# Performance work log

Measured on AMD Instinct MI355X. Metric: run time of the kernel, lower is better.

The kernel has to match this reference:

```python
import jax, jax.numpy as jnp
import numpy as np

N_NODES = 50000
HEADS = 4
OUT_DIM = 64
NEG_SLOPE = 0.2
BETA = 0.5
C_CONST = 1.0
EPS = 1e-16


def setup_inputs() -> dict:
    key = jax.random.key(0)
    ks = jax.random.split(key, 6)
    in_dim = 128
    x = jax.random.normal(ks[0], (N_NODES, in_dim), dtype=jnp.float32)
    edge_index = jax.random.randint(ks[1], (2, 800000), 0, N_NODES, dtype=jnp.int64)
    # GATConv params (glorot-ish scale)
    W = jax.random.normal(ks[2], (in_dim, HEADS * OUT_DIM), dtype=jnp.float32) * (1.0 / np.sqrt(in_dim))
    att_src = jax.random.normal(ks[3], (HEADS, OUT_DIM), dtype=jnp.float32) * (1.0 / np.sqrt(OUT_DIM))
    att_dst = jax.random.normal(ks[4], (HEADS, OUT_DIM), dtype=jnp.float32) * (1.0 / np.sqrt(OUT_DIM))
    bias = jnp.zeros((HEADS * OUT_DIM,), dtype=jnp.float32)
    return {"x": x, "edge_index": edge_index, "W": W, "att_src": att_src,
            "att_dst": att_dst, "bias": bias}


def _gat_conv(x, edge_index, W, att_src, att_dst, bias):
    N = x.shape[0]
    # add self loops (PyG GATConv default)
    loop = jnp.arange(N, dtype=edge_index.dtype)
    src = jnp.concatenate([edge_index[0], loop])
    dst = jnp.concatenate([edge_index[1], loop])
    # linear transform: [N, H, F]
    h = (x @ W).reshape(N, HEADS, OUT_DIM)
    # per-node attention logits: [N, H]
    a_src = jnp.einsum('nhf,hf->nh', h, att_src)
    a_dst = jnp.einsum('nhf,hf->nh', h, att_dst)
    # per-edge logits and segment softmax over destination nodes
    e = jax.nn.leaky_relu(a_src[src] + a_dst[dst], negative_slope=NEG_SLOPE)  # [E, H]
    m = jax.ops.segment_max(e, dst, num_segments=N)                           # [N, H]
    ex = jnp.exp(e - m[dst])
    s = jax.ops.segment_sum(ex, dst, num_segments=N)                          # [N, H]
    alpha = ex / (s[dst] + EPS)                                               # [E, H]
    # aggregate messages: [N, H, F]
    out = jax.ops.segment_sum(alpha[:, :, None] * h[src], dst, num_segments=N)
    return out.reshape(N, HEADS * OUT_DIM) + bias


def reference(x, edge_index, W, att_src, att_dst, bias):
    # eval mode: feature dropout and attention dropout are identity
    z = _gat_conv(x, edge_index, W, att_src, att_dst, bias)
    return BETA * z + (C_CONST - BETA) * jax.nn.elu(z)
```

## Files before the change

### kernel.cpp

```cpp
#include <hip/hip_runtime.h>
#include <hip/hip_bf16.h>

typedef unsigned short u16;
typedef __attribute__((ext_vector_type(8))) short bf16x8;
typedef __attribute__((ext_vector_type(4))) float f32x4;

#define HEADS 4
#define OUT_DIM 64
#define HF 256
#define IN_DIM 128
#define NEG_SLOPE 0.2f
#define EPSF 1e-16f

__device__ __forceinline__ float braw2f(u16 u) {
    union { float f; unsigned int i; } c; c.i = ((unsigned int)u) << 16; return c.f;
}
__device__ __forceinline__ u16 f2braw(float v) {
    __hip_bfloat16 t = __float2bfloat16(v);
    return *(u16*)&t;
}
__device__ __forceinline__ float lrelu(float e) { return e < 0.f ? NEG_SLOPE * e : e; }

__device__ __forceinline__ bool detect_i64(const int* ei) {
    return (ei[1] | ei[3] | ei[5] | ei[7] | ei[9] | ei[11] | ei[13] | ei[15]) == 0;
}
__device__ __forceinline__ void get_edge(const int* ei, int E, int t, bool i64,
                                         int& s, int& d) {
    if (t < E) {
        if (i64) { s = ei[2 * t]; d = ei[2 * (E + t)]; }
        else     { s = ei[t];     d = ei[E + t]; }
    } else {
        s = d = t - E;
    }
}

__global__ __launch_bounds__(256) void init_kernel(const float* __restrict__ W,
                                                   const float* __restrict__ att_s,
                                                   const float* __restrict__ att_d,
                                                   float* __restrict__ wa_s,
                                                   float* __restrict__ wa_d,
                                                   int* __restrict__ cnt4,
                                                   int* __restrict__ cur,
                                                   int* __restrict__ gcnt,
                                                   int* __restrict__ hist,
                                                   int* __restrict__ bcur,
                                                   int N, int NZ) {
    int b = blockIdx.x;
    if (b == 0) {
        if (threadIdx.x == 0) *gcnt = 0;
        hist[threadIdx.x] = 0;
        bcur[threadIdx.x] = 0;
    }
    if (b < NZ) {
        int i = b * 256 + threadIdx.x;
        if (i < N) {
            cnt4[i] = 0;
            cnt4[N + i] = 0;
            cnt4[2 * N + i] = 0;
            cnt4[3 * N + i] = 0;
            cur[i] = 0;
        }
    } else {
        for (int idx = threadIdx.x; idx < HEADS * IN_DIM; idx += 256) {
            int h = idx >> 7, k = idx & 127;
            float ss = 0.f, sd = 0.f;
            for (int f = 0; f < OUT_DIM; ++f) {
                float wv = W[k * HF + h * OUT_DIM + f];
                ss = fmaf(wv, att_s[h * OUT_DIM + f], ss);
                sd = fmaf(wv, att_d[h * OUT_DIM + f], sd);
            }
            wa_s[idx] = ss;
            wa_d[idx] = sd;
        }
    }
}

__global__ __launch_bounds__(256) void phase1_kernel(const float* __restrict__ x,
                                                     const int* __restrict__ ei,
                                                     const float* __restrict__ W,
                                                     const float* __restrict__ wa_s,
                                                     const float* __restrict__ wa_d,
                                                     float* __restrict__ a_src,
                                                     float* __restrict__ a_dst,
                                                     u16* __restrict__ xb,
                                                     u16* __restrict__ Wfrag,
                                                     int* __restrict__ cnt4,
                                                     int N, int E, int NA, int NC) {
    int b = blockIdx.x;
    if (b < NA) {
        int wid = threadIdx.x >> 6;
        int l = threadIdx.x & 63;
        int g = l >> 4, c = l & 15, kc = c * 8;
        int v = b * 16 + wid * 4 + g;
        if (v >= N) return;

        const float4* xr = (const float4*)(x + (size_t)v * IN_DIM + kc);
        float4 x0 = xr[0], x1 = xr[1];

        uint4 u;
        u.x = (unsigned)f2braw(x0.x) | ((unsigned)f2braw(x0.y) << 16);
        u.y = (unsigned)f2braw(x0.z) | ((unsigned)f2braw(x0.w) << 16);
        u.z = (unsigned)f2braw(x1.x) | ((unsigned)f2braw(x1.y) << 16);
        u.w = (unsigned)f2braw(x1.z) | ((unsigned)f2braw(x1.w) << 16);
        *(uint4*)(xb + (size_t)v * IN_DIM + kc) = u;

        float ps[4], pd[4];
        #pragma unroll
        for (int h = 0; h < 4; ++h) {
            const float4* s4 = (const float4*)(wa_s + h * IN_DIM + kc);
            const float4* d4 = (const float4*)(wa_d + h * IN_DIM + kc);
            float4 s0 = s4[0], s1 = s4[1], d0 = d4[0], d1 = d4[1];
            ps[h] = x0.x*s0.x + x0.y*s0.y + x0.z*s0.z + x0.w*s0.w
                  + x1.x*s1.x + x1.y*s1.y + x1.z*s1.z + x1.w*s1.w;
            pd[h] = x0.x*d0.x + x0.y*d0.y + x0.z*d0.z + x0.w*d0.w
                  + x1.x*d1.x + x1.y*d1.y + x1.z*d1.z + x1.w*d1.w;
        }
        #pragma unroll
        for (int off = 1; off < 16; off <<= 1) {
            #pragma unroll
            for (int h = 0; h < 4; ++h) {
                ps[h] += __shfl_xor(ps[h], off);
                pd[h] += __shfl_xor(pd[h], off);
            }
        }
        if (c == 0) {
            float4 vs, vd;
            vs.x = ps[0]; vs.y = ps[1]; vs.z = ps[2]; vs.w = ps[3];
            vd.x = pd[0]; vd.y = pd[1]; vd.z = pd[2]; vd.w = pd[3];
            *(float4*)(a_src + (size_t)v * HEADS) = vs;
            *(float4*)(a_dst + (size_t)v * HEADS) = vd;
        }
    } else if (b < NA + NC) {
        int t = (b - NA) * 256 + threadIdx.x;
        if (t >= E + N) return;
        bool i64 = detect_i64(ei);
        int src, dst; get_edge(ei, E, t, i64, src, dst);
        if (src >= 0 && src < N && dst >= 0 && dst < N)
            atomicAdd(cnt4 + (t & 3) * N + dst, 1);
    } else {
        int bb = b - NA - NC;
        for (int idx = bb * 256 + threadIdx.x; idx < 32768; idx += 8 * 256) {
            int j = idx & 7, l = (idx >> 3) & 63, t = (idx >> 9) & 3;
            int s = (idx >> 11) & 3, h = (idx >> 13) & 3;
            int k = s * 32 + ((l >> 4) & 3) * 8 + j;
            int col = h * OUT_DIM + t * 16 + (l & 15);
            Wfrag[idx] = f2braw(W[k * HF + col]);
        }
    }
}

__global__ __launch_bounds__(256) void offset_kernel(int* __restrict__ cnt4,
                                                     int* __restrict__ offs,
                                                     int* __restrict__ gcnt,
                                                     int* __restrict__ hist, int N) {
    __shared__ int lh[256];
    lh[threadIdx.x] = 0;
    __syncthreads();

    int idx = blockIdx.x * 256 + threadIdx.x;
    int l = threadIdx.x & 63;
    int d = 0;
    if (idx < N) {
        d = cnt4[idx] + cnt4[N + idx] + cnt4[2 * N + idx] + cnt4[3 * N + idx];
        cnt4[idx] = d;
        atomicAdd(lh + min(max(d, 0), 255), 1);
    }

    int s = d;
    #pragma unroll
    for (int off = 1; off < 64; off <<= 1) {
        int t = __shfl_up(s, off);
        if (l >= off) s += t;
    }
    int base = 0;
    if (l == 63) base = atomicAdd(gcnt, s);
    base = __shfl(base, 63);
    if (idx < N) offs[idx] = base + s - d;

    __syncthreads();
    if (lh[threadIdx.x]) atomicAdd(hist + threadIdx.x, lh[threadIdx.x]);
}

__global__ __launch_bounds__(256) void fillscatter_kernel(const int* __restrict__ ei,
                                                          const int* __restrict__ offs,
                                                          int* __restrict__ cur,
                                                          int* __restrict__ slots,
                                                          uint2* __restrict__ wslots,
                                                          const float* __restrict__ a_src,
                                                          const float* __restrict__ a_dst,
                                                          const int* __restrict__ cnt,
                                                          const int* __restrict__ hist,
                                                          int* __restrict__ bcur,
                                                          int* __restrict__ perm,
                                                          int E, int N, int NC) {
    __shared__ int sc[256];
    __shared__ int lh[256];
    __shared__ int lbase[256];

    int b = blockIdx.x;
    if (b < NC) {
        int t = b * 256 + threadIdx.x;
        if (t >= E + N) return;
        bool i64 = detect_i64(ei);
        int src, dst; get_edge(ei, E, t, i64, src, dst);
        if (src >= 0 && src < N && dst >= 0 && dst < N) {
            int pos = atomicAdd(cur + dst, 1);
            int idx = offs[dst] + pos;
            slots[idx] = src;
            if (wslots) {
                float4 as = ((const float4*)a_src)[src];
                float4 ad = ((const float4*)a_dst)[dst];
                float w0 = __expf(lrelu(as.x + ad.x));
                float w1 = __expf(lrelu(as.y + ad.y));
                float w2 = __expf(lrelu(as.z + ad.z));
                float w3 = __expf(lrelu(as.w + ad.w));
                uint2 wp;
                wp.x = (unsigned)f2braw(w0) | ((unsigned)f2braw(w1) << 16);
                wp.y = (unsigned)f2braw(w2) | ((unsigned)f2braw(w3) << 16);
                wslots[idx] = wp;
            }
        }
    } else {
        int tid = threadIdx.x;
        sc[tid] = hist[tid];
        lh[tid] = 0;
        __syncthreads();
        #pragma unroll
        for (int off = 1; off < 256; off <<= 1) {
            int tv = (tid >= off) ? sc[tid - off] : 0;
            __syncthreads();
            sc[tid] += tv;
            __syncthreads();
        }

        int idx = (b - NC) * 256 + tid;
        int bk = 0, mypos = 0;
        bool valid = (idx < N);
        if (valid) {
            bk = min(max(cnt[idx], 0), 255);
            mypos = atomicAdd(lh + bk, 1);
        }
        __syncthreads();
        int c = lh[tid];
        if (c) lbase[tid] = atomicAdd(bcur + tid, c);
        __syncthreads();
        if (valid) {
            int p = (N - sc[bk]) + lbase[bk] + mypos;
            if (p >= 0 && p < N) perm[p] = idx;
        }
    }
}

#define ACC_EDGE(wp, r) do { \
    float w0_ = braw2f((wp).x & 0xffff), w1_ = braw2f((wp).x >> 16); \
    float w2_ = braw2f((wp).y & 0xffff), w3_ = braw2f((wp).y >> 16); \
    ls0 += w0_; ls1 += w1_; ls2 += w2_; ls3 += w3_; \
    float xv_[8]; \
    xv_[0] = braw2f((r).x & 0xffff); xv_[1] = braw2f((r).x >> 16); \
    xv_[2] = braw2f((r).y & 0xffff); xv_[3] = braw2f((r).y >> 16); \
    xv_[4] = braw2f((r).z & 0xffff); xv_[5] = braw2f((r).z >> 16); \
    xv_[6] = braw2f((r).w & 0xffff); xv_[7] = braw2f((r).w >> 16); \
    _Pragma("unroll") \
    for (int q_ = 0; q_ < 8; ++q_) { \
        G0[q_] = fmaf(w0_, xv_[q_], G0[q_]); \
        G1[q_] = fmaf(w1_, xv_[q_], G1[q_]); \
        G2[q_] = fmaf(w2_, xv_[q_], G2[q_]); \
        G3[q_] = fmaf(w3_, xv_[q_], G3[q_]); \
    } \
} while (0)

__global__ __launch_bounds__(256) void fused_gz_kernel(const int* __restrict__ perm,
                                                       const int* __restrict__ offs,
                                                       const int* __restrict__ cnt,
                                                       const int* __restrict__ slots,
                                                       const uint2* __restrict__ wslots,
                                                       const u16* __restrict__ xb,
                                                       const u16* __restrict__ Wfrag,
                                                       const float* __restrict__ bias,
                                                       float* __restrict__ out,
                                                       int N, int ET) {
    __shared__ u16 smem[16 * 520];
    __shared__ int pvals[16];

    int tid = threadIdx.x;
    int wid = tid >> 6;
    int l = tid & 63;
    int g = l >> 4, c = l & 15, kc = c * 8;
    int n = wid * 4 + g;
    int pidx = blockIdx.x * 16 + n;

    int v = -1;
    if (pidx < N) {
        v = perm[pidx];
        if (v < 0 || v >= N) v = -1;
    }
    if (c == 0) pvals[n] = v;

    int beg = 0, end = 0;
    if (v >= 0) {
        beg = offs[v];
        int deg = cnt[v];
        beg = max(0, min(beg, ET));
        end = max(beg, min(beg + deg, ET));
    }

    float ls0 = 0.f, ls1 = 0.f, ls2 = 0.f, ls3 = 0.f;
    float G0[8] = {0,0,0,0,0,0,0,0};
    float G1[8] = {0,0,0,0,0,0,0,0};
    float G2[8] = {0,0,0,0,0,0,0,0};
    float G3[8] = {0,0,0,0,0,0,0,0};

    int j = beg;
    for (; j + 4 <= end; j += 4) {
        int s0 = max(0, min(slots[j],     N - 1));
        int s1 = max(0, min(slots[j + 1], N - 1));
        int s2 = max(0, min(slots[j + 2], N - 1));
        int s3 = max(0, min(slots[j + 3], N - 1));
        uint2 wp0 = wslots[j];
        uint2 wp1 = wslots[j + 1];
        uint2 wp2 = wslots[j + 2];
        uint2 wp3 = wslots[j + 3];
        uint4 r0 = *(const uint4*)(xb + (size_t)s0 * IN_DIM + kc);
        uint4 r1 = *(const uint4*)(xb + (size_t)s1 * IN_DIM + kc);
        uint4 r2 = *(const uint4*)(xb + (size_t)s2 * IN_DIM + kc);
        uint4 r3 = *(const uint4*)(xb + (size_t)s3 * IN_DIM + kc);
        ACC_EDGE(wp0, r0);
        ACC_EDGE(wp1, r1);
        ACC_EDGE(wp2, r2);
        ACC_EDGE(wp3, r3);
    }
    for (; j < end; ++j) {
        int s0 = max(0, min(slots[j], N - 1));
        uint2 wp0 = wslots[j];
        uint4 r0 = *(const uint4*)(xb + (size_t)s0 * IN_DIM + kc);
        ACC_EDGE(wp0, r0);
    }

    if (v >= 0) {
        float i0 = 1.f / (ls0 + EPSF), i1 = 1.f / (ls1 + EPSF);
        float i2 = 1.f / (ls2 + EPSF), i3 = 1.f / (ls3 + EPSF);
        u16* lp = smem + n * 520 + c * 8;
        #pragma unroll
        for (int h = 0; h < 4; ++h) {
            const float* G = h == 0 ? G0 : h == 1 ? G1 : h == 2 ? G2 : G3;
            float inv = h == 0 ? i0 : h == 1 ? i1 : h == 2 ? i2 : i3;
            uint4 u;
            u.x = (unsigned)f2braw(G[0] * inv) | ((unsigned)f2braw(G[1] * inv) << 16);
            u.y = (unsigned)f2braw(G[2] * inv) | ((unsigned)f2braw(G[3] * inv) << 16);
            u.z = (unsigned)f2braw(G[4] * inv) | ((unsigned)f2braw(G[5] * inv) << 16);
            u.w = (unsigned)f2braw(G[6] * inv) | ((unsigned)f2braw(G[7] * inv) << 16);
            *(uint4*)(lp + h * 128) = u;
        }
    } else {
        u16* lp = smem + n * 520 + c * 8;
        uint4 z = {0, 0, 0, 0};
        #pragma unroll
        for (int h = 0; h < 4; ++h) *(uint4*)(lp + h * 128) = z;
    }
    __syncthreads();

    int h = wid;
    int q = l >> 4, mcol = l & 15;

    const u16* lp = smem + mcol * 520 + h * 128 + q * 8;
    bf16x8 A[4];
    A[0] = *(const bf16x8*)(lp);
    A[1] = *(const bf16x8*)(lp + 32);
    A[2] = *(const bf16x8*)(lp + 64);
    A[3] = *(const bf16x8*)(lp + 96);

    f32x4 acc0 = {0.f,0.f,0.f,0.f}, acc1 = acc0, acc2 = acc0, acc3 = acc0;
    #pragma unroll
    for (int s = 0; s < 4; ++s) {
        const u16* wb = Wfrag + (((h * 4 + s) * 4) << 9) + l * 8;
        bf16x8 B0 = *(const bf16x8*)(wb);
        bf16x8 B1 = *(const bf16x8*)(wb + 512);
        bf16x8 B2 = *(const bf16x8*)(wb + 1024);
        bf16x8 B3 = *(const bf16x8*)(wb + 1536);
        acc0 = __builtin_amdgcn_mfma_f32_16x16x32_bf16(A[s], B0, acc0, 0, 0, 0);
        acc1 = __builtin_amdgcn_mfma_f32_16x16x32_bf16(A[s], B1, acc1, 0, 0, 0);
        acc2 = __builtin_amdgcn_mfma_f32_16x16x32_bf16(A[s], B2, acc2, 0, 0, 0);
        acc3 = __builtin_amdgcn_mfma_f32_16x16x32_bf16(A[s], B3, acc3, 0, 0, 0);
    }

    #pragma unroll
    for (int bt = 0; bt < 4; ++bt) {
        f32x4 a = bt == 0 ? acc0 : bt == 1 ? acc1 : bt == 2 ? acc2 : acc3;
        float b = bias[h * OUT_DIM + bt * 16 + mcol];
        #pragma unroll
        for (int r = 0; r < 4; ++r) {
            int vv = pvals[q * 4 + r];
            if (vv >= 0) {
                float z = a[r] + b;
                float y = z > 0.f ? z : 0.5f * z + 0.5f * (__expf(z) - 1.f);
                out[(size_t)vv * HF + h * OUT_DIM + bt * 16 + mcol] = y;
            }
        }
    }
}

__global__ __launch_bounds__(512) void gather_bf_kernel(const int* __restrict__ offs,
                                                        const int* __restrict__ cnt,
                                                        const int* __restrict__ slots,
                                                        const u16* __restrict__ xb,
                                                        const float* __restrict__ a_src,
                                                        const float* __restrict__ a_dst,
                                                        u16* __restrict__ Gout, int N, int ET) {
    int v = (blockIdx.x * 512 + threadIdx.x) >> 6;
    int l = threadIdx.x & 63;
    if (v >= N) return;
    int h = l >> 4, c = l & 15, kc = c * 8;

    int beg = offs[v];
    int deg = cnt[v];
    beg = max(0, min(beg, ET));
    int end = max(beg, min(beg + deg, ET));
    float adh = a_dst[v * HEADS + h];

    float ls = 0.f;
    float G[8] = {0.f,0.f,0.f,0.f,0.f,0.f,0.f,0.f};

    int j = beg;
    for (; j + 4 <= end; j += 4) {
        int s0 = max(0, min(slots[j],     N - 1));
        int s1 = max(0, min(slots[j + 1], N - 1));
        int s2 = max(0, min(slots[j + 2], N - 1));
        int s3 = max(0, min(slots[j + 3], N - 1));
        float w0 = __expf(lrelu(a_src[s0 * HEADS + h] + adh));
        float w1 = __expf(lrelu(a_src[s1 * HEADS + h] + adh));
        float w2 = __expf(lrelu(a_src[s2 * HEADS + h] + adh));
        float w3 = __expf(lrelu(a_src[s3 * HEADS + h] + adh));
        uint4 r0 = *(const uint4*)(xb + (size_t)s0 * IN_DIM + kc);
        uint4 r1 = *(const uint4*)(xb + (size_t)s1 * IN_DIM + kc);
        uint4 r2 = *(const uint4*)(xb + (size_t)s2 * IN_DIM + kc);
        uint4 r3 = *(const uint4*)(xb + (size_t)s3 * IN_DIM + kc);
        ls += (w0 + w1) + (w2 + w3);
        unsigned ua[4];
        ua[0]=r0.x; ua[1]=r0.y; ua[2]=r0.z; ua[3]=r0.w;
        #pragma unroll
        for (int q = 0; q < 4; ++q) {
            G[2*q]   = fmaf(w0, braw2f(ua[q] & 0xffff), G[2*q]);
            G[2*q+1] = fmaf(w0, braw2f(ua[q] >> 16),    G[2*q+1]);
        }
        ua[0]=r1.x; ua[1]=r1.y; ua[2]=r1.z; ua[3]=r1.w;
        #pragma unroll
        for (int q = 0; q < 4; ++q) {
            G[2*q]   = fmaf(w1, braw2f(ua[q] & 0xffff), G[2*q]);
            G[2*q+1] = fmaf(w1, braw2f(ua[q] >> 16),    G[2*q+1]);
        }
        ua[0]=r2.x; ua[1]=r2.y; ua[2]=r2.z; ua[3]=r2.w;
        #pragma unroll
        for (int q = 0; q < 4; ++q) {
            G[2*q]   = fmaf(w2, braw2f(ua[q] & 0xffff), G[2*q]);
            G[2*q+1] = fmaf(w2, braw2f(ua[q] >> 16),    G[2*q+1]);
        }
        ua[0]=r3.x; ua[1]=r3.y; ua[2]=r3.z; ua[3]=r3.w;
        #pragma unroll
        for (int q = 0; q < 4; ++q) {
            G[2*q]   = fmaf(w3, braw2f(ua[q] & 0xffff), G[2*q]);
            G[2*q+1] = fmaf(w3, braw2f(ua[q] >> 16),    G[2*q+1]);
        }
    }
    for (; j < end; ++j) {
        int s0 = max(0, min(slots[j], N - 1));
        float w0 = __expf(lrelu(a_src[s0 * HEADS + h] + adh));
        uint4 r0 = *(const uint4*)(xb + (size_t)s0 * IN_DIM + kc);
        ls += w0;
        unsigned ua[4]; ua[0]=r0.x; ua[1]=r0.y; ua[2]=r0.z; ua[3]=r0.w;
        #pragma unroll
        for (int q = 0; q < 4; ++q) {
            G[2*q]   = fmaf(w0, braw2f(ua[q] & 0xffff), G[2*q]);
            G[2*q+1] = fmaf(w0, braw2f(ua[q] >> 16),    G[2*q+1]);
        }
    }

    float inv = 1.f / (ls + EPSF);
    uint4 u;
    u.x = (unsigned)f2braw(G[0] * inv) | ((unsigned)f2braw(G[1] * inv) << 16);
    u.y = (unsigned)f2braw(G[2] * inv) | ((unsigned)f2braw(G[3] * inv) << 16);
    u.z = (unsigned)f2braw(G[4] * inv) | ((unsigned)f2braw(G[5] * inv) << 16);
    u.w = (unsigned)f2braw(G[6] * inv) | ((unsigned)f2braw(G[7] * inv) << 16);
    *(uint4*)(Gout + (size_t)v * 512 + h * 128 + kc) = u;
}

__global__ __launch_bounds__(512) void gather_f32_kernel(const int* __restrict__ offs,
                                                         const int* __restrict__ cnt,
                                                         const int* __restrict__ slots,
                                                         const float* __restrict__ x,
                                                         const float* __restrict__ a_src,
                                                         const float* __restrict__ a_dst,
                                                         u16* __restrict__ Gout, int N, int ET) {
    int v = (blockIdx.x * 512 + threadIdx.x) >> 6;
    int l = threadIdx.x & 63;
    if (v >= N) return;
    int h = l >> 4, c = l & 15, kc = c * 8;

    int beg = offs[v];
    int deg = cnt[v];
    beg = max(0, min(beg, ET));
    int end = max(beg, min(beg + deg, ET));
    float adh = a_dst[v * HEADS + h];

    float ls = 0.f;
    float G[8] = {0.f,0.f,0.f,0.f,0.f,0.f,0.f,0.f};
    for (int j = beg; j < end; ++j) {
        int s0 = max(0, min(slots[j], N - 1));
        float w0 = __expf(lrelu(a_src[s0 * HEADS + h] + adh));
        const float4* xr0 = (const float4*)(x + (size_t)s0 * IN_DIM + kc);
        float4 a0 = xr0[0], b0 = xr0[1];
        ls += w0;
        G[0]=fmaf(w0,a0.x,G[0]); G[1]=fmaf(w0,a0.y,G[1]);
        G[2]=fmaf(w0,a0.z,G[2]); G[3]=fmaf(w0,a0.w,G[3]);
        G[4]=fmaf(w0,b0.x,G[4]); G[5]=fmaf(w0,b0.y,G[5]);
        G[6]=fmaf(w0,b0.z,G[6]); G[7]=fmaf(w0,b0.w,G[7]);
    }
    float inv = 1.f / (ls + EPSF);
    uint4 u;
    u.x = (unsigned)f2braw(G[0] * inv) | ((unsigned)f2braw(G[1] * inv) << 16);
    u.y = (unsigned)f2braw(G[2] * inv) | ((unsigned)f2braw(G[3] * inv) << 16);
    u.z = (unsigned)f2braw(G[4] * inv) | ((unsigned)f2braw(G[5] * inv) << 16);
    u.w = (unsigned)f2braw(G[6] * inv) | ((unsigned)f2braw(G[7] * inv) << 16);
    *(uint4*)(Gout + (size_t)v * 512 + h * 128 + kc) = u;
}

__global__ __launch_bounds__(256) void zgemm_kernel(const u16* __restrict__ Wfrag,
                                                    const float* __restrict__ bias,
                                                    float* __restrict__ out, int N) {
    int h = threadIdx.x >> 6;
    int l = threadIdx.x & 63;
    int q = l >> 4, mcol = l & 15;
    int nb = blockIdx.x * 16;

    const u16* G = (const u16*)out;
    bool valid = (nb + mcol) < N;
    int vA = valid ? nb + mcol : N - 1;
    const u16* gp = G + (size_t)vA * 512 + h * 128 + q * 8;
    bf16x8 A[4];
    A[0] = *(const bf16x8*)(gp);
    A[1] = *(const bf16x8*)(gp + 32);
    A[2] = *(const bf16x8*)(gp + 64);
    A[3] = *(const bf16x8*)(gp + 96);
    if (!valid) {
        bf16x8 zz = {0,0,0,0,0,0,0,0};
        A[0] = zz; A[1] = zz; A[2] = zz; A[3] = zz;
    }

    f32x4 acc0 = {0.f,0.f,0.f,0.f}, acc1 = acc0, acc2 = acc0, acc3 = acc0;
    #pragma unroll
    for (int s = 0; s < 4; ++s) {
        const u16* wb = Wfrag + (((h * 4 + s) * 4) << 9) + l * 8;
        bf16x8 B0 = *(const bf16x8*)(wb);
        bf16x8 B1 = *(const bf16x8*)(wb + 512);
        bf16x8 B2 = *(const bf16x8*)(wb + 1024);
        bf16x8 B3 = *(const bf16x8*)(wb + 1536);
        acc0 = __builtin_amdgcn_mfma_f32_16x16x32_bf16(A[s], B0, acc0, 0, 0, 0);
        acc1 = __builtin_amdgcn_mfma_f32_16x16x32_bf16(A[s], B1, acc1, 0, 0, 0);
        acc2 = __builtin_amdgcn_mfma_f32_16x16x32_bf16(A[s], B2, acc2, 0, 0, 0);
        acc3 = __builtin_amdgcn_mfma_f32_16x16x32_bf16(A[s], B3, acc3, 0, 0, 0);
    }

    #pragma unroll
    for (int t = 0; t < 4; ++t) {
        f32x4 a = t == 0 ? acc0 : t == 1 ? acc1 : t == 2 ? acc2 : acc3;
        float b = bias[h * OUT_DIM + t * 16 + mcol];
        #pragma unroll
        for (int r = 0; r < 4; ++r) {
            int v = nb + q * 4 + r;
            if (v < N) {
                float z = a[r] + b;
                float y = z > 0.f ? z : 0.5f * z + 0.5f * (__expf(z) - 1.f);
                out[(size_t)v * HF + h * OUT_DIM + t * 16 + mcol] = y;
            }
        }
    }
}

extern "C" void kernel_launch(void* const* d_in, const int* in_sizes, int n_in,
                              void* d_out, int out_size, void* d_ws, size_t ws_size,
                              hipStream_t stream) {
    const float* x       = (const float*)d_in[0];
    const int*   ei      = (const int*)d_in[1];
    const float* W       = (const float*)d_in[2];
    const float* att_src = (const float*)d_in[3];
    const float* att_dst = (const float*)d_in[4];
    const float* bias    = (const float*)d_in[5];

    const int N = in_sizes[0] / IN_DIM;
    const int E = in_sizes[1] / 2;
    const int ET = E + N;
    const int NT = (N + 255) / 256;

    char* ws = (char*)d_ws;
    size_t off = 0;
    float* wa_s   = (float*)(ws + off); off += HEADS * IN_DIM * 4;
    float* wa_d   = (float*)(ws + off); off += HEADS * IN_DIM * 4;
    u16*   Wfrag  = (u16*)(ws + off);   off += 32768 * 2;
    float* a_src  = (float*)(ws + off); off += (size_t)N * HEADS * 4;
    float* a_dst  = (float*)(ws + off); off += (size_t)N * HEADS * 4;
    int*   offs   = (int*)(ws + off);   off += ((size_t)N * 4 + 15) & ~(size_t)15;
    int*   cnt4   = (int*)(ws + off);   off += ((size_t)N * 16 + 15) & ~(size_t)15;
    int*   cur    = (int*)(ws + off);   off += ((size_t)N * 4 + 15) & ~(size_t)15;
    int*   gcnt   = (int*)(ws + off);   off += 64;
    int*   hist   = (int*)(ws + off);   off += 256 * 4;
    int*   bcur   = (int*)(ws + off);   off += 256 * 4;
    int*   perm   = (int*)(ws + off);   off += ((size_t)N * 4 + 15) & ~(size_t)15;
    int*   slots  = (int*)(ws + off);   off += ((size_t)ET * 4 + 15) & ~(size_t)15;
    u16*   xb     = (u16*)(ws + off);   size_t need_bf = off + (size_t)N * IN_DIM * 2;
    uint2* wslots = (uint2*)(ws + need_bf);
    size_t need_w = need_bf + (size_t)ET * 8;
    bool use_bf = (ws_size >= need_bf);
    bool use_w  = (ws_size >= need_w);

    const int NA = (N + 15) / 16;
    const int NC = (ET + 255) / 256;

    init_kernel<<<NT + 1, 256, 0, stream>>>(W, att_src, att_dst, wa_s, wa_d,
                                            cnt4, cur, gcnt, hist, bcur, N, NT);
    phase1_kernel<<<NA + NC + 8, 256, 0, stream>>>(x, ei, W, wa_s, wa_d, a_src, a_dst,
                                                   use_bf ? xb : (u16*)d_out,
                                                   Wfrag, cnt4, N, E, NA, NC);
    offset_kernel<<<NT, 256, 0, stream>>>(cnt4, offs, gcnt, hist, N);
    fillscatter_kernel<<<NC + (use_w ? NT : 0), 256, 0, stream>>>(
        ei, offs, cur, slots, use_w ? wslots : (uint2*)0, a_src, a_dst,
        cnt4, hist, bcur, perm, E, N, NC);
    if (use_w) {
        fused_gz_kernel<<<(N + 15) / 16, 256, 0, stream>>>(perm, offs, cnt4, slots,
                                                           wslots, xb, Wfrag, bias,
                                                           (float*)d_out, N, ET);
    } else if (use_bf) {
        gather_bf_kernel<<<(N * 64 + 511) / 512, 512, 0, stream>>>(offs, cnt4, slots, xb,
                                                                   a_src, a_dst,
                                                                   (u16*)d_out, N, ET);
        zgemm_kernel<<<(N + 15) / 16, 256, 0, stream>>>(Wfrag, bias, (float*)d_out, N);
    } else {
        gather_f32_kernel<<<(N * 64 + 511) / 512, 512, 0, stream>>>(offs, cnt4, slots, x,
                                                                    a_src, a_dst,
                                                                    (u16*)d_out, N, ET);
        zgemm_kernel<<<(N + 15) / 16, 256, 0, stream>>>(Wfrag, bias, (float*)d_out, N);
    }
}
```

Baseline: 260.1 us.

## Split each node's edge loop across two wave groups in fused gather-GEMM kernel

Doubles the block size of the fused gather+GEMM kernel to 512 threads. Each destination node's edge list is now split between two groups of four waves, and the second group's partial sums are reduced through shared memory before normalization and the MFMA projection. The aim is to halve the per-thread serial gather latency and expose more memory-level parallelism. In exchange it adds shared-memory traffic, two extra barriers, more LDS per block, and idle waves during the GEMM phase.

```diff
diff --git a/kernel.cpp b/kernel.cpp
--- a/kernel.cpp
+++ b/kernel.cpp
@@ -269,7 +269,7 @@
     } \
 } while (0)
 
-__global__ __launch_bounds__(256) void fused_gz_kernel(const int* __restrict__ perm,
+__global__ __launch_bounds__(512) void fused_gz_kernel(const int* __restrict__ perm,
                                                        const int* __restrict__ offs,
                                                        const int* __restrict__ cnt,
                                                        const int* __restrict__ slots,
@@ -279,14 +279,18 @@
                                                        const float* __restrict__ bias,
                                                        float* __restrict__ out,
                                                        int N, int ET) {
-    __shared__ u16 smem[16 * 520];
+    __shared__ float pG[16 * 528];
+    __shared__ float lsP[16][4];
     __shared__ int pvals[16];
+    u16* smem = (u16*)pG;
 
     int tid = threadIdx.x;
     int wid = tid >> 6;
+    int role = wid >> 2;
+    int wsub = wid & 3;
     int l = tid & 63;
     int g = l >> 4, c = l & 15, kc = c * 8;
-    int n = wid * 4 + g;
+    int n = wsub * 4 + g;
     int pidx = blockIdx.x * 16 + n;
 
     int v = -1;
@@ -294,14 +298,18 @@
         v = perm[pidx];
         if (v < 0 || v >= N) v = -1;
     }
-    if (c == 0) pvals[n] = v;
-
-    int beg = 0, end = 0;
+    if (role == 0 && c == 0) pvals[n] = v;
+
+    int jbeg = 0, jend = 0;
     if (v >= 0) {
-        beg = offs[v];
+        int beg = offs[v];
         int deg = cnt[v];
         beg = max(0, min(beg, ET));
-        end = max(beg, min(beg + deg, ET));
+        int end = max(beg, min(beg + deg, ET));
+        deg = end - beg;
+        int h1 = min(deg, ((deg >> 1) + 3) & ~3);
+        jbeg = role == 0 ? beg : beg + h1;
+        jend = role == 0 ? beg + h1 : end;
     }
 
     float ls0 = 0.f, ls1 = 0.f, ls2 = 0.f, ls3 = 0.f;
@@ -310,8 +318,8 @@
     float G2[8] = {0,0,0,0,0,0,0,0};
     float G3[8] = {0,0,0,0,0,0,0,0};
 
-    int j = beg;
-    for (; j + 4 <= end; j += 4) {
+    int j = jbeg;
+    for (; j + 4 <= jend; j += 4) {
         int s0 = max(0, min(slots[j],     N - 1));
         int s1 = max(0, min(slots[j + 1], N - 1));
         int s2 = max(0, min(slots[j + 2], N - 1));
@@ -329,71 +337,106 @@
         ACC_EDGE(wp2, r2);
         ACC_EDGE(wp3, r3);
     }
-    for (; j < end; ++j) {
+    for (; j < jend; ++j) {
         int s0 = max(0, min(slots[j], N - 1));
         uint2 wp0 = wslots[j];
         uint4 r0 = *(const uint4*)(xb + (size_t)s0 * IN_DIM + kc);
         ACC_EDGE(wp0, r0);
     }
 
-    if (v >= 0) {
-        float i0 = 1.f / (ls0 + EPSF), i1 = 1.f / (ls1 + EPSF);
-        float i2 = 1.f / (ls2 + EPSF), i3 = 1.f / (ls3 + EPSF);
+    if (role == 1 && v >= 0) {
+        float* p = pG + n * 528 + c * 33;
+        #pragma unroll
+        for (int q = 0; q < 8; ++q) p[q] = G0[q];
+        #pragma unroll
+        for (int q = 0; q < 8; ++q) p[8 + q] = G1[q];
+        #pragma unroll
+        for (int q = 0; q < 8; ++q) p[16 + q] = G2[q];
+        #pragma unroll
+        for (int q = 0; q < 8; ++q) p[24 + q] = G3[q];
+        if (c == 0) {
+            lsP[n][0] = ls0; lsP[n][1] = ls1;
+            lsP[n][2] = ls2; lsP[n][3] = ls3;
+        }
+    }
+    __syncthreads();
+
+    if (role == 0 && v >= 0) {
+        const float* p = pG + n * 528 + c * 33;
+        #pragma unroll
+        for (int q = 0; q < 8; ++q) G0[q] += p[q];
+        #pragma unroll
+        for (int q = 0; q < 8; ++q) G1[q] += p[8 + q];
+        #pragma unroll
+        for (int q = 0; q < 8; ++q) G2[q] += p[16 + q];
+        #pragma unroll
+        for (int q = 0; q < 8; ++q) G3[q] += p[24 + q];
+        ls0 += lsP[n][0]; ls1 += lsP[n][1];
+        ls2 += lsP[n][2]; ls3 += lsP[n][3];
+    }
+    __syncthreads();
+
+    if (role == 0) {
         u16* lp = smem + n * 520 + c * 8;
-        #pragma unroll
-        for (int h = 0; h < 4; ++h) {
-            const float* G = h == 0 ? G0 : h == 1 ? G1 : h == 2 ? G2 : G3;
-            float inv = h == 0 ? i0 : h == 1 ? i1 : h == 2 ? i2 : i3;
-            uint4 u;
-            u.x = (unsigned)f2braw(G[0] * inv) | ((unsigned)f2braw(G[1] * inv) << 16);
-            u.y = (unsigned)f2braw(G[2] * inv) | ((unsigned)f2braw(G[3] * inv) << 16);
-            u.z = (unsigned)f2braw(G[4] * inv) | ((unsigned)f2braw(G[5] * inv) << 16);
-            u.w = (unsigned)f2braw(G[6] * inv) | ((unsigned)f2braw(G[7] * inv) << 16);
-            *(uint4*)(lp + h * 128) = u;
-        }
-    } else {
-        u16* lp = smem + n * 520 + c * 8;
-        uint4 z = {0, 0, 0, 0};
-        #pragma unroll
-        for (int h = 0; h < 4; ++h) *(uint4*)(lp + h * 128) = z;
+        if (v >= 0) {
+            float i0 = 1.f / (ls0 + EPSF), i1 = 1.f / (ls1 + EPSF);
+            float i2 = 1.f / (ls2 + EPSF), i3 = 1.f / (ls3 + EPSF);
+            #pragma unroll
+            for (int h = 0; h < 4; ++h) {
+                const float* G = h == 0 ? G0 : h == 1 ? G1 : h == 2 ? G2 : G3;
+                float inv = h == 0 ? i0 : h == 1 ? i1 : h == 2 ? i2 : i3;
+                uint4 u;
+                u.x = (unsigned)f2braw(G[0] * inv) | ((unsigned)f2braw(G[1] * inv) << 16);
+                u.y = (unsigned)f2braw(G[2] * inv) | ((unsigned)f2braw(G[3] * inv) << 16);
+                u.z = (unsigned)f2braw(G[4] * inv) | ((unsigned)f2braw(G[5] * inv) << 16);
+                u.w = (unsigned)f2braw(G[6] * inv) | ((unsigned)f2braw(G[7] * inv) << 16);
+                *(uint4*)(lp + h * 128) = u;
+            }
+        } else {
+            uint4 z = {0, 0, 0, 0};
+            #pragma unroll
+            for (int h = 0; h < 4; ++h) *(uint4*)(lp + h * 128) = z;
+        }
     }
     __syncthreads();
 
-    int h = wid;
-    int q = l >> 4, mcol = l & 15;
-
-    const u16* lp = smem + mcol * 520 + h * 128 + q * 8;
-    bf16x8 A[4];
-    A[0] = *(const bf16x8*)(lp);
-    A[1] = *(const bf16x8*)(lp + 32);
-    A[2] = *(const bf16x8*)(lp + 64);
-    A[3] = *(const bf16x8*)(lp + 96);
-
-    f32x4 acc0 = {0.f,0.f,0.f,0.f}, acc1 = acc0, acc2 = acc0, acc3 = acc0;
-    #pragma unroll
-    for (int s = 0; s < 4; ++s) {
-        const u16* wb = Wfrag + (((h * 4 + s) * 4) << 9) + l * 8;
-        bf16x8 B0 = *(const bf16x8*)(wb);
-        bf16x8 B1 = *(const bf16x8*)(wb + 512);
-        bf16x8 B2 = *(const bf16x8*)(wb + 1024);
-        bf16x8 B3 = *(const bf16x8*)(wb + 1536);
-        acc0 = __builtin_amdgcn_mfma_f32_16x16x32_bf16(A[s], B0, acc0, 0, 0, 0);
-        acc1 = __builtin_amdgcn_mfma_f32_16x16x32_bf16(A[s], B1, acc1, 0, 0, 0);
-        acc2 = __builtin_amdgcn_mfma_f32_16x16x32_bf16(A[s], B2, acc2, 0, 0, 0);
-        acc3 = __builtin_amdgcn_mfma_f32_16x16x32_bf16(A[s], B3, acc3, 0, 0, 0);
-    }
-
-    #pragma unroll
-    for (int bt = 0; bt < 4; ++bt) {
-        f32x4 a = bt == 0 ? acc0 : bt == 1 ? acc1 : bt == 2 ? acc2 : acc3;
-        float b = bias[h * OUT_DIM + bt * 16 + mcol];
-        #pragma unroll
-        for (int r = 0; r < 4; ++r) {
-            int vv = pvals[q * 4 + r];
-            if (vv >= 0) {
-                float z = a[r] + b;
-                float y = z > 0.f ? z : 0.5f * z + 0.5f * (__expf(z) - 1.f);
-                out[(size_t)vv * HF + h * OUT_DIM + bt * 16 + mcol] = y;
+    if (wid < 4) {
+        int h = wid;
+        int q = l >> 4, mcol = l & 15;
+
+        const u16* lp = smem + mcol * 520 + h * 128 + q * 8;
+        bf16x8 A[4];
+        A[0] = *(const bf16x8*)(lp);
+        A[1] = *(const bf16x8*)(lp + 32);
+        A[2] = *(const bf16x8*)(lp + 64);
+        A[3] = *(const bf16x8*)(lp + 96);
+
+        f32x4 acc0 = {0.f,0.f,0.f,0.f}, acc1 = acc0, acc2 = acc0, acc3 = acc0;
+        #pragma unroll
+        for (int s = 0; s < 4; ++s) {
+            const u16* wb = Wfrag + (((h * 4 + s) * 4) << 9) + l * 8;
+            bf16x8 B0 = *(const bf16x8*)(wb);
+            bf16x8 B1 = *(const bf16x8*)(wb + 512);
+            bf16x8 B2 = *(const bf16x8*)(wb + 1024);
+            bf16x8 B3 = *(const bf16x8*)(wb + 1536);
+            acc0 = __builtin_amdgcn_mfma_f32_16x16x32_bf16(A[s], B0, acc0, 0, 0, 0);
+            acc1 = __builtin_amdgcn_mfma_f32_16x16x32_bf16(A[s], B1, acc1, 0, 0, 0);
+            acc2 = __builtin_amdgcn_mfma_f32_16x16x32_bf16(A[s], B2, acc2, 0, 0, 0);
+            acc3 = __builtin_amdgcn_mfma_f32_16x16x32_bf16(A[s], B3, acc3, 0, 0, 0);
+        }
+
+        #pragma unroll
+        for (int bt = 0; bt < 4; ++bt) {
+            f32x4 a = bt == 0 ? acc0 : bt == 1 ? acc1 : bt == 2 ? acc2 : acc3;
+            float b = bias[h * OUT_DIM + bt * 16 + mcol];
+            #pragma unroll
+            for (int r = 0; r < 4; ++r) {
+                int vv = pvals[q * 4 + r];
+                if (vv >= 0) {
+                    float z = a[r] + b;
+                    float y = z > 0.f ? z : 0.5f * z + 0.5f * (__expf(z) - 1.f);
+                    out[(size_t)vv * HF + h * OUT_DIM + bt * 16 + mcol] = y;
+                }
             }
         }
     }
@@ -624,7 +667,7 @@
         ei, offs, cur, slots, use_w ? wslots : (uint2*)0, a_src, a_dst,
         cnt4, hist, bcur, perm, E, N, NC);
     if (use_w) {
-        fused_gz_kernel<<<(N + 15) / 16, 256, 0, stream>>>(perm, offs, cnt4, slots,
+        fused_gz_kernel<<<(N + 15) / 16, 512, 0, stream>>>(perm, offs, cnt4, slots,
                                                            wslots, xb, Wfrag, bias,
                                                            (float*)d_out, N, ET);
     } else if (use_bf) {
```

Result: slower. 266.8 us (+2.6%).
